# Performance work log

Hardware: AMD Instinct MI355X
Metric: run time of the kernel (lower is better)

The kernel has to match this reference:

```python
import jax, jax.numpy as jnp
import numpy as np

N_SRC0, N_DST0 = 100000, 20000   # block0: 100k src -> 20k dst
N_DST1 = 4096                    # block1: 20k src -> 4096 dst (seed nodes)


def setup_inputs() -> dict:
    key = jax.random.key(0)
    ks = jax.random.split(key, 8)
    E0, E1 = 640000, 131072
    return {
        "features": jax.random.normal(ks[0], (N_SRC0, 256), jnp.float32),
        "W1": jax.random.normal(ks[1], (256, 256), jnp.float32) * (1.0 / np.sqrt(256)),
        "b1": jnp.zeros((256,), jnp.float32),
        "W2": jax.random.normal(ks[2], (256, 128), jnp.float32) * (1.0 / np.sqrt(256)),
        "b2": jnp.zeros((128,), jnp.float32),
        "src0": jax.random.randint(ks[3], (E0,), 0, N_SRC0, jnp.int32),
        "dst0": jax.random.randint(ks[4], (E0,), 0, N_DST0, jnp.int32),
        "src1": jax.random.randint(ks[5], (E1,), 0, N_DST0, jnp.int32),
        "dst1": jax.random.randint(ks[6], (E1,), 0, N_DST1, jnp.int32),
    }


def _graph_conv(src, dst, n_dst, feat, W, b):
    # DGL GraphConv, norm='both': D_out^{-1/2} gather-sum D_in^{-1/2}, then WX+b.
    n_src = feat.shape[0]
    ones = jnp.ones(src.shape[0], feat.dtype)
    out_deg = jax.ops.segment_sum(ones, src, num_segments=n_src)
    norm_src = jnp.clip(out_deg, 1.0, None) ** -0.5          # [n_src]
    h = feat * norm_src[:, None]
    agg = jax.ops.segment_sum(h[src], dst, num_segments=n_dst)  # sparse SpMM
    in_deg = jax.ops.segment_sum(ones, dst, num_segments=n_dst)
    norm_dst = jnp.clip(in_deg, 1.0, None) ** -0.5           # [n_dst]
    return (agg * norm_dst[:, None]) @ W + b


def reference(features, W1, b1, W2, b2, src0, dst0, src1, dst1):
    x = jax.nn.relu(_graph_conv(src0, dst0, N_DST0, features, W1, b1))
    x = _graph_conv(src1, dst1, N_DST1, x, W2, b2)
    return x
```

## Files before the change

### kernel.cpp

```cpp
#include <hip/hip_runtime.h>
#include <hip/hip_bf16.h>

#define K_DIM 256
#define RSTRIDE 128
#define EPB 8192

#define G0_DB 625
#define G0_SB 256
#define G0_SW 392
#define G1_DB 128
#define G1_SB 64
#define G1_SW 313

#define NB_FIN (G0_DB + G1_DB + G0_SB + G1_SB)
#define CAST_BLKS 2048

typedef short bf16x8 __attribute__((ext_vector_type(8)));
typedef float f32x4 __attribute__((ext_vector_type(4)));

static __device__ __forceinline__ unsigned short f2bf(float x) {
    __hip_bfloat16 b = __float2bfloat16(x);
    return *reinterpret_cast<unsigned short*>(&b);
}
static __device__ __forceinline__ float bflo(unsigned int p) {
    return __uint_as_float(p << 16);
}
static __device__ __forceinline__ float bfhi(unsigned int p) {
    return __uint_as_float(p & 0xffff0000u);
}

static __device__ __forceinline__ void block_exscan(
        const int* __restrict__ hist, int* __restrict__ offs, int* __restrict__ tmp, int M) {
    const int tid = threadIdx.x;
    const int S = (M + 255) >> 8;
    const int base = tid * S;
    int sum = 0;
    for (int k = 0; k < S; ++k) {
        int idx = base + k;
        if (idx < M) sum += hist[idx];
    }
    tmp[tid] = sum;
    __syncthreads();
    for (int d = 1; d < 256; d <<= 1) {
        int v = tmp[tid];
        int u = (tid >= d) ? tmp[tid - d] : 0;
        __syncthreads();
        tmp[tid] = v + u;
        __syncthreads();
    }
    int run = (tid == 0) ? 0 : tmp[tid - 1];
    for (int k = 0; k < S; ++k) {
        int idx = base + k;
        if (idx < M) { offs[idx] = run; run += hist[idx]; }
    }
    __syncthreads();
}

struct SplitSh {
    int hist[640];
    int offs[640];
    int tmp[256];
    unsigned sorted[EPB];
};

template <int NDB, int NSB, int SW>
static __device__ __forceinline__ void split_sort(
        const int* __restrict__ src, const int* __restrict__ dst, int E, int chunk,
        int* __restrict__ cntD, int* __restrict__ offD,
        int* __restrict__ cntS, int* __restrict__ offS,
        unsigned* __restrict__ sortD, unsigned* __restrict__ sortS, SplitSh& sh) {
    const int tid = threadIdx.x;
    const int e0 = chunk * EPB;
    const int n = min(EPB, E - e0);
    for (int i = tid; i < NDB; i += 256) sh.hist[i] = 0;
    __syncthreads();
    for (int j = tid; j < n; j += 256) atomicAdd(&sh.hist[dst[e0 + j] >> 5], 1);
    __syncthreads();
    block_exscan(sh.hist, sh.offs, sh.tmp, NDB);
    for (int i = tid; i < NDB; i += 256) {
        cntD[chunk * NDB + i] = sh.hist[i];
        offD[chunk * NDB + i] = sh.offs[i];
    }
    __syncthreads();
    for (int j = tid; j < n; j += 256) {
        int d = dst[e0 + j];
        int s = src[e0 + j];
        int pos = atomicAdd(&sh.offs[d >> 5], 1);
        sh.sorted[pos] = ((unsigned)s << 5) | (unsigned)(d & 31);
    }
    __syncthreads();
    {
        unsigned* __restrict__ gout = sortD + (size_t)chunk * EPB;
        for (int j = tid; j < n; j += 256) gout[j] = sh.sorted[j];
    }
    __syncthreads();
    for (int i = tid; i < NSB; i += 256) sh.hist[i] = 0;
    __syncthreads();
    for (int j = tid; j < n; j += 256)
        atomicAdd(&sh.hist[(int)((unsigned)src[e0 + j] / SW)], 1);
    __syncthreads();
    block_exscan(sh.hist, sh.offs, sh.tmp, NSB);
    for (int i = tid; i < NSB; i += 256) {
        cntS[chunk * NSB + i] = sh.hist[i];
        offS[chunk * NSB + i] = sh.offs[i];
    }
    __syncthreads();
    for (int j = tid; j < n; j += 256) {
        unsigned s = (unsigned)src[e0 + j];
        int pos = atomicAdd(&sh.offs[s / SW], 1);
        sh.sorted[pos] = s;
    }
    __syncthreads();
    {
        unsigned* __restrict__ gout = sortS + (size_t)chunk * EPB;
        for (int j = tid; j < n; j += 256) gout[j] = sh.sorted[j];
    }
}

__global__ __launch_bounds__(256) void splitA_kernel(
        const int* __restrict__ src0, const int* __restrict__ dst0, int E0,
        const int* __restrict__ src1, const int* __restrict__ dst1, int E1,
        int* __restrict__ cntD0, int* __restrict__ offD0,
        int* __restrict__ cntS0, int* __restrict__ offS0,
        unsigned* __restrict__ sortD0, unsigned* __restrict__ sortS0,
        int* __restrict__ cntD1, int* __restrict__ offD1,
        int* __restrict__ cntS1, int* __restrict__ offS1,
        unsigned* __restrict__ sortD1, unsigned* __restrict__ sortS1,
        int nA0, int nA1,
        const float* __restrict__ W1, uint4* __restrict__ pw1,
        const float* __restrict__ W2, uint4* __restrict__ pw2) {
    __shared__ SplitSh sh;
    const int b = blockIdx.x;
    if (b < nA0) {
        split_sort<G0_DB, G0_SB, G0_SW>(src0, dst0, E0, b,
                                        cntD0, offD0, cntS0, offS0, sortD0, sortS0, sh);
    } else if (b < nA0 + nA1) {
        split_sort<G1_DB, G1_SB, G1_SW>(src1, dst1, E1, b - nA0,
                                        cntD1, offD1, cntS1, offS1, sortD1, sortS1, sh);
    } else if (b < nA0 + nA1 + 32) {
        int idx = (b - nA0 - nA1) * blockDim.x + threadIdx.x;
        int lane = idx & 63;
        int kt = (idx >> 6) & 7;
        int nt = idx >> 9;
        int n = nt * 16 + (lane & 15);
        int k = kt * 32 + (lane >> 4) * 8;
        union { unsigned short us[8]; uint4 u; } o;
#pragma unroll
        for (int j = 0; j < 8; ++j) o.us[j] = f2bf(W1[(size_t)(k + j) * 256 + n]);
        pw1[idx] = o.u;
    } else {
        int idx = (b - nA0 - nA1 - 32) * blockDim.x + threadIdx.x;
        int lane = idx & 63;
        int kt = (idx >> 6) & 7;
        int nt = idx >> 9;
        int n = nt * 16 + (lane & 15);
        int k = kt * 32 + (lane >> 4) * 8;
        union { unsigned short us[8]; uint4 u; } o;
#pragma unroll
        for (int j = 0; j < 8; ++j) o.us[j] = f2bf(W2[(size_t)(k + j) * 128 + n]);
        pw2[idx] = o.u;
    }
}

template <int NDB, int GT>
static __device__ __forceinline__ void fin_dst(
        const unsigned* __restrict__ sortD, const int* __restrict__ cntD,
        const int* __restrict__ offD, int nblk, int b,
        int* __restrict__ esrc, int* __restrict__ cnt, int* tile, int* rowc) {
    const int tid = threadIdx.x;
    if (tid < 32) rowc[tid] = 0;
    __syncthreads();
    for (int rr = tid / GT; rr < nblk; rr += 256 / GT) {
        const int c = cntD[rr * NDB + b];
        const int o = offD[rr * NDB + b];
        const unsigned* __restrict__ seg = sortD + (size_t)rr * EPB + o;
        for (int j = tid % GT; j < c; j += GT) {
            unsigned v = seg[j];
            int dloc = v & 31;
            int s = (int)(v >> 5);
            int slot = atomicAdd(&rowc[dloc], 1);
            if (slot < RSTRIDE) tile[(dloc << 7) + slot] = s;
        }
    }
    __syncthreads();
    int* __restrict__ gout = esrc + ((size_t)b << 12);
    for (int i = tid; i < 32 * RSTRIDE; i += 256) gout[i] = tile[i];
    if (tid < 32) cnt[b * 32 + tid] = rowc[tid];
}

template <int NSB, int SW, int GT>
static __device__ __forceinline__ void fin_src(
        const unsigned* __restrict__ sortS, const int* __restrict__ cntS,
        const int* __restrict__ offS, int nblk, int b, int NN,
        float* __restrict__ nv, int* hist) {
    const int tid = threadIdx.x;
    for (int i = tid; i < SW; i += 256) hist[i] = 0;
    __syncthreads();
    const int base = b * SW;
    for (int rr = tid / GT; rr < nblk; rr += 256 / GT) {
        const int c = cntS[rr * NSB + b];
        const int o = offS[rr * NSB + b];
        const unsigned* __restrict__ seg = sortS + (size_t)rr * EPB + o;
        for (int j = tid % GT; j < c; j += GT)
            atomicAdd(&hist[(int)seg[j] - base], 1);
    }
    __syncthreads();
    for (int i = tid; i < SW; i += 256) {
        int node = base + i;
        if (node < NN) nv[node] = rsqrtf((float)max(hist[i], 1));
    }
}

__global__ __launch_bounds__(256) void castfin_kernel(
        int nA0, int nA1,
        const unsigned* __restrict__ sortD0, const int* __restrict__ cntD0,
        const int* __restrict__ offD0, int* __restrict__ cnt0, int* __restrict__ esrc0,
        const unsigned* __restrict__ sortD1, const int* __restrict__ cntD1,
        const int* __restrict__ offD1, int* __restrict__ cnt1, int* __restrict__ esrc1,
        const unsigned* __restrict__ sortS0, const int* __restrict__ cntS0,
        const int* __restrict__ offS0, float* __restrict__ nv0,
        const unsigned* __restrict__ sortS1, const int* __restrict__ cntS1,
        const int* __restrict__ offS1, float* __restrict__ nv1,
        const float* __restrict__ feat, unsigned short* __restrict__ h, int numVec) {
    __shared__ union {
        struct { int tile[32 * RSTRIDE]; int rowc[32]; } d;
        int hist[G0_SW];
    } sh;
    int b = blockIdx.x;
    if (b < G0_DB) {
        fin_dst<G0_DB, 2>(sortD0, cntD0, offD0, nA0, b, esrc0, cnt0, sh.d.tile, sh.d.rowc);
    } else if (b < G0_DB + G1_DB) {
        fin_dst<G1_DB, 16>(sortD1, cntD1, offD1, nA1, b - G0_DB, esrc1, cnt1,
                           sh.d.tile, sh.d.rowc);
    } else if (b < G0_DB + G1_DB + G0_SB) {
        fin_src<G0_SB, G0_SW, 2>(sortS0, cntS0, offS0, nA0, b - G0_DB - G1_DB,
                                 100000, nv0, sh.hist);
    } else if (b < NB_FIN) {
        fin_src<G1_SB, G1_SW, 16>(sortS1, cntS1, offS1, nA1, b - G0_DB - G1_DB - G0_SB,
                                  20000, nv1, sh.hist);
    } else {
        for (int v = (b - NB_FIN) * 256 + (int)threadIdx.x; v < numVec;
             v += CAST_BLKS * 256) {
            const int idx = v * 8;
            const float4 v0 = *reinterpret_cast<const float4*>(feat + idx);
            const float4 v1 = *reinterpret_cast<const float4*>(feat + idx + 4);
            union { ushort4 u4[2]; uint4 u; } o;
            o.u4[0].x = f2bf(v0.x); o.u4[0].y = f2bf(v0.y);
            o.u4[0].z = f2bf(v0.z); o.u4[0].w = f2bf(v0.w);
            o.u4[1].x = f2bf(v1.x); o.u4[1].y = f2bf(v1.y);
            o.u4[1].z = f2bf(v1.z); o.u4[1].w = f2bf(v1.w);
            *reinterpret_cast<uint4*>(h + idx) = o.u;
        }
    }
}

template <bool NORM>
static __device__ __forceinline__ void gather2_to_lds(
        const unsigned short* __restrict__ hfeat, const int* __restrict__ esrc,
        const int* __restrict__ cnt, const float* __restrict__ nv,
        int m0, int w, int lane, unsigned short (*Alds)[264]) {
#pragma unroll
    for (int k = 0; k < 2; ++k) {
        const int rloc = w * 2 + k;
        const int row = m0 + rloc;
        const int c = cnt[row];
        const int cend = min(c, RSTRIDE);
        const int* __restrict__ ep = esrc + ((size_t)row << 7);
        float a0 = 0.f, a1 = 0.f, a2 = 0.f, a3 = 0.f;
        int i = 0;
        for (; i + 7 < cend; i += 8) {
            int s[8];
            uint2 p[8];
            float nn[8];
#pragma unroll
            for (int u = 0; u < 8; ++u) s[u] = ep[i + u];
#pragma unroll
            for (int u = 0; u < 8; ++u)
                p[u] = *reinterpret_cast<const uint2*>(hfeat + (((size_t)s[u]) << 8) + lane * 4);
#pragma unroll
            for (int u = 0; u < 8; ++u)
                nn[u] = NORM ? nv[s[u]] : 1.0f;
#pragma unroll
            for (int u = 0; u < 8; ++u) {
                if (NORM) {
                    a0 = fmaf(bflo(p[u].x), nn[u], a0); a1 = fmaf(bfhi(p[u].x), nn[u], a1);
                    a2 = fmaf(bflo(p[u].y), nn[u], a2); a3 = fmaf(bfhi(p[u].y), nn[u], a3);
                } else {
                    a0 += bflo(p[u].x); a1 += bfhi(p[u].x);
                    a2 += bflo(p[u].y); a3 += bfhi(p[u].y);
                }
            }
        }
        for (; i < cend; ++i) {
            int s0 = ep[i];
            float n0 = NORM ? nv[s0] : 1.0f;
            const uint2 p0 = *reinterpret_cast<const uint2*>(hfeat + (((size_t)s0) << 8) + lane * 4);
            if (NORM) {
                a0 = fmaf(bflo(p0.x), n0, a0); a1 = fmaf(bfhi(p0.x), n0, a1);
                a2 = fmaf(bflo(p0.y), n0, a2); a3 = fmaf(bfhi(p0.y), n0, a3);
            } else {
                a0 += bflo(p0.x); a1 += bfhi(p0.x);
                a2 += bflo(p0.y); a3 += bfhi(p0.y);
            }
        }
        float nd = rsqrtf((float)max(c, 1));
        ushort4 o;
        o.x = f2bf(a0 * nd);
        o.y = f2bf(a1 * nd);
        o.z = f2bf(a2 * nd);
        o.w = f2bf(a3 * nd);
        *reinterpret_cast<ushort4*>(&Alds[rloc][lane * 4]) = o;
    }
}

__global__ __launch_bounds__(512, 8) void fused0_kernel(
        const unsigned short* __restrict__ hfeat, const int* __restrict__ esrc,
        const int* __restrict__ cnt, const float* __restrict__ nv0,
        const uint4* __restrict__ pW, const float* __restrict__ bias,
        const float* __restrict__ nv1, unsigned short* __restrict__ out) {
    __shared__ unsigned short Alds[16][264];
    const int m0 = blockIdx.x * 16;
    const int w = threadIdx.x >> 6;
    const int lane = threadIdx.x & 63;
    gather2_to_lds<true>(hfeat, esrc, cnt, nv0, m0, w, lane, Alds);
    __syncthreads();

    bf16x8 a[8];
    const unsigned short* ap = &Alds[lane & 15][(lane >> 4) * 8];
#pragma unroll
    for (int kt = 0; kt < 8; ++kt)
        a[kt] = *reinterpret_cast<const bf16x8*>(ap + kt * 32);

    const int rbase = m0 + (lane >> 4) * 4;
    float nsv[4];
#pragma unroll
    for (int r = 0; r < 4; ++r) nsv[r] = nv1[rbase + r];

#pragma unroll
    for (int nt = 0; nt < 2; ++nt) {
        const int n0 = w * 32 + nt * 16;
        f32x4 acc = {0.f, 0.f, 0.f, 0.f};
#pragma unroll
        for (int kt = 0; kt < 8; ++kt) {
            bf16x8 b = *reinterpret_cast<const bf16x8*>(&pW[((size_t)(n0 >> 4) * 8 + kt) * 64 + lane]);
            acc = __builtin_amdgcn_mfma_f32_16x16x32_bf16(a[kt], b, acc, 0, 0, 0);
        }
        const int col = n0 + (lane & 15);
        const float bv = bias[col];
#pragma unroll
        for (int r = 0; r < 4; ++r) {
            float v = fmaxf(acc[r] + bv, 0.0f) * nsv[r];
            out[(size_t)(rbase + r) * K_DIM + col] = f2bf(v);
        }
    }
}

__global__ __launch_bounds__(512, 8) void fused1_kernel(
        const unsigned short* __restrict__ xb, const int* __restrict__ esrc,
        const int* __restrict__ cnt,
        const uint4* __restrict__ pW, const float* __restrict__ bias,
        float* __restrict__ out) {
    __shared__ unsigned short Alds[16][264];
    const int m0 = blockIdx.x * 16;
    const int w = threadIdx.x >> 6;
    const int lane = threadIdx.x & 63;
    gather2_to_lds<false>(xb, esrc, cnt, nullptr, m0, w, lane, Alds);
    __syncthreads();

    bf16x8 a[8];
    const unsigned short* ap = &Alds[lane & 15][(lane >> 4) * 8];
#pragma unroll
    for (int kt = 0; kt < 8; ++kt)
        a[kt] = *reinterpret_cast<const bf16x8*>(ap + kt * 32);

    const int rbase = m0 + (lane >> 4) * 4;
    {
        const int n0 = w * 16;
        f32x4 acc = {0.f, 0.f, 0.f, 0.f};
#pragma unroll
        for (int kt = 0; kt < 8; ++kt) {
            bf16x8 b = *reinterpret_cast<const bf16x8*>(&pW[((size_t)(n0 >> 4) * 8 + kt) * 64 + lane]);
            acc = __builtin_amdgcn_mfma_f32_16x16x32_bf16(a[kt], b, acc, 0, 0, 0);
        }
        const int col = n0 + (lane & 15);
        const float bv = bias[col];
#pragma unroll
        for (int r = 0; r < 4; ++r)
            out[(size_t)(rbase + r) * 128 + col] = acc[r] + bv;
    }
}

__global__ __launch_bounds__(256) void gatherf_kernel(
        const float* __restrict__ feat, const int* __restrict__ esrc,
        const int* __restrict__ cnt, const int* __restrict__ od,
        float* __restrict__ outbuf, int n_dst) {
    int row = blockIdx.x * (blockDim.x >> 6) + (threadIdx.x >> 6);
    int lane = threadIdx.x & 63;
    if (row >= n_dst) return;
    const int c = cnt[row];
    const int cend = min(c, RSTRIDE);
    const int* __restrict__ ep = esrc + ((size_t)row << 7);
    float4 acc = {0.f, 0.f, 0.f, 0.f};
    for (int i = 0; i < cend; ++i) {
        int s0 = ep[i];
        float n0 = rsqrtf((float)max(od[s0], 1));
        const float4 v0 = *reinterpret_cast<const float4*>(feat + (((size_t)s0) << 8) + lane * 4);
        acc.x = fmaf(v0.x, n0, acc.x); acc.y = fmaf(v0.y, n0, acc.y);
        acc.z = fmaf(v0.z, n0, acc.z); acc.w = fmaf(v0.w, n0, acc.w);
    }
    float nd = rsqrtf((float)max(c, 1));
    float4 o = {acc.x * nd, acc.y * nd, acc.z * nd, acc.w * nd};
    *reinterpret_cast<float4*>(outbuf + (((size_t)row) << 8) + lane * 4) = o;
}

__global__ void edges_kernel(const int* __restrict__ src0, const int* __restrict__ dst0,
                             int* __restrict__ od0, int* __restrict__ cnt0,
                             int* __restrict__ esrc0, int E0,
                             const int* __restrict__ src1, const int* __restrict__ dst1,
                             int* __restrict__ od1, int* __restrict__ cnt1,
                             int* __restrict__ esrc1, int E1) {
    int i = blockIdx.x * blockDim.x + threadIdx.x;
    if (i < E0) {
        int s = src0[i];
        int d = dst0[i];
        atomicAdd(&od0[s], 1);
        int slot = atomicAdd(&cnt0[d], 1);
        if (slot < RSTRIDE) esrc0[(d << 7) + slot] = s;
    } else if (i < E0 + E1) {
        int e = i - E0;
        int s = src1[e];
        int d = dst1[e];
        atomicAdd(&od1[s], 1);
        int slot = atomicAdd(&cnt1[d], 1);
        if (slot < RSTRIDE) esrc1[(d << 7) + slot] = s;
    }
}

template <int ROWS, int NCOLS, bool RELU>
__global__ __launch_bounds__(NCOLS) void gemm_kernel(
        const float* __restrict__ A, const float* __restrict__ W,
        const float* __restrict__ bias, float* __restrict__ out, int M) {
    const int row0 = blockIdx.x * ROWS;
    const int c = threadIdx.x;
    const float* __restrict__ Ablk = A + (size_t)row0 * K_DIM;
    const float* __restrict__ Wc = W + c;

    float acc[ROWS];
#pragma unroll
    for (int r = 0; r < ROWS; ++r) acc[r] = 0.0f;

    float w0 = Wc[0];
    float w1 = Wc[NCOLS];
    float w2 = Wc[2 * NCOLS];
    float w3 = Wc[3 * NCOLS];

#pragma unroll 2
    for (int k = 0; k < K_DIM - 4; k += 4) {
        const float* p = Wc + (size_t)(k + 4) * NCOLS;
        float n0 = p[0];
        float n1 = p[NCOLS];
        float n2 = p[2 * NCOLS];
        float n3 = p[3 * NCOLS];
#pragma unroll
        for (int r = 0; r < ROWS; ++r) {
            const float4 a = *reinterpret_cast<const float4*>(Ablk + r * K_DIM + k);
            acc[r] = fmaf(a.x, w0, acc[r]);
            acc[r] = fmaf(a.y, w1, acc[r]);
            acc[r] = fmaf(a.z, w2, acc[r]);
            acc[r] = fmaf(a.w, w3, acc[r]);
        }
        w0 = n0; w1 = n1; w2 = n2; w3 = n3;
    }
    {
        const int k = K_DIM - 4;
#pragma unroll
        for (int r = 0; r < ROWS; ++r) {
            const float4 a = *reinterpret_cast<const float4*>(Ablk + r * K_DIM + k);
            acc[r] = fmaf(a.x, w0, acc[r]);
            acc[r] = fmaf(a.y, w1, acc[r]);
            acc[r] = fmaf(a.z, w2, acc[r]);
            acc[r] = fmaf(a.w, w3, acc[r]);
        }
    }

    const float b = bias[c];
#pragma unroll
    for (int r = 0; r < ROWS; ++r) {
        float v = acc[r] + b;
        if (RELU) v = fmaxf(v, 0.0f);
        out[(size_t)(row0 + r) * NCOLS + c] = v;
    }
}

extern "C" void kernel_launch(void* const* d_in, const int* in_sizes, int n_in,
                              void* d_out, int out_size, void* d_ws, size_t ws_size,
                              hipStream_t stream) {
    const float* features = (const float*)d_in[0];
    const float* W1 = (const float*)d_in[1];
    const float* b1 = (const float*)d_in[2];
    const float* W2 = (const float*)d_in[3];
    const float* b2 = (const float*)d_in[4];
    const int* src0 = (const int*)d_in[5];
    const int* dst0 = (const int*)d_in[6];
    const int* src1 = (const int*)d_in[7];
    const int* dst1 = (const int*)d_in[8];
    const int E0 = in_sizes[5];
    const int E1 = in_sizes[7];
    const int NSRC0 = 100000, NDST0 = 20000, NDST1 = 4096;
    const int nA0 = (E0 + EPB - 1) / EPB;
    const int nA1 = (E1 + EPB - 1) / EPB;

    char* ws = (char*)d_ws;
    size_t off = 0;
    auto carve = [&](size_t bytes) -> void* {
        void* p = ws + off;
        off = (off + bytes + 255) & ~(size_t)255;
        return p;
    };
    int* od0  = (int*)carve((size_t)NSRC0 * 4);
    int* od1  = (int*)carve((size_t)NDST0 * 4);
    int* cnt0 = (int*)carve((size_t)NDST0 * 4);
    int* cnt1 = (int*)carve((size_t)NDST1 * 4);
    const size_t zero_span = off;
    int* esrc0p = (int*)carve((size_t)NDST0 * RSTRIDE * 4);
    int* esrc1p = (int*)carve((size_t)NDST1 * RSTRIDE * 4);
    uint4* pW1  = (uint4*)carve((size_t)8192 * 16);
    uint4* pW2  = (uint4*)carve((size_t)4096 * 16);
    int* cntD0 = (int*)carve((size_t)nA0 * G0_DB * 4);
    int* offD0 = (int*)carve((size_t)nA0 * G0_DB * 4);
    int* cntS0 = (int*)carve((size_t)nA0 * G0_SB * 4);
    int* offS0 = (int*)carve((size_t)nA0 * G0_SB * 4);
    int* cntD1 = (int*)carve((size_t)nA1 * G1_DB * 4);
    int* offD1 = (int*)carve((size_t)nA1 * G1_DB * 4);
    int* cntS1 = (int*)carve((size_t)nA1 * G1_SB * 4);
    int* offS1 = (int*)carve((size_t)nA1 * G1_SB * 4);
    unsigned* sortD0 = (unsigned*)carve((size_t)nA0 * EPB * 4);
    unsigned* sortS0 = (unsigned*)carve((size_t)nA0 * EPB * 4);
    unsigned* sortD1 = (unsigned*)carve((size_t)nA1 * EPB * 4);
    unsigned* sortS1 = (unsigned*)carve((size_t)nA1 * EPB * 4);
    unsigned short* xbufb = (unsigned short*)carve((size_t)NDST0 * K_DIM * 2);
    unsigned short* hfeat = (unsigned short*)carve((size_t)NSRC0 * K_DIM * 2);
    const size_t need_bf16 = off;
    (void)n_in; (void)out_size;

    if (ws_size >= need_bf16) {
        float* nv0 = (float*)od0;
        float* nv1 = (float*)od1;
        const int numVec = NSRC0 * K_DIM / 8;
        splitA_kernel<<<nA0 + nA1 + 48, 256, 0, stream>>>(
            src0, dst0, E0, src1, dst1, E1,
            cntD0, offD0, cntS0, offS0, sortD0, sortS0,
            cntD1, offD1, cntS1, offS1, sortD1, sortS1,
            nA0, nA1, W1, pW1, W2, pW2);
        castfin_kernel<<<NB_FIN + CAST_BLKS, 256, 0, stream>>>(
            nA0, nA1,
            sortD0, cntD0, offD0, cnt0, esrc0p,
            sortD1, cntD1, offD1, cnt1, esrc1p,
            sortS0, cntS0, offS0, nv0,
            sortS1, cntS1, offS1, nv1,
            features, hfeat, numVec);
        fused0_kernel<<<NDST0 / 16, 512, 0, stream>>>(
            hfeat, esrc0p, cnt0, nv0, pW1, b1, nv1, xbufb);
        fused1_kernel<<<NDST1 / 16, 512, 0, stream>>>(
            xbufb, esrc1p, cnt1, pW2, b2, (float*)d_out);
    } else {
        hipMemsetAsync(ws, 0, zero_span, stream);
        float* agg0 = (float*)carve((size_t)NDST0 * K_DIM * 4);
        float* xbuf = (float*)carve((size_t)NDST0 * K_DIM * 4);
        float* agg1 = (float*)carve((size_t)NDST1 * K_DIM * 4);
        edges_kernel<<<(E0 + E1 + 255) / 256, 256, 0, stream>>>(
            src0, dst0, od0, cnt0, esrc0p, E0,
            src1, dst1, od1, cnt1, esrc1p, E1);
        gatherf_kernel<<<(NDST0 + 3) / 4, 256, 0, stream>>>(features, esrc0p, cnt0, od0,
                                                            agg0, NDST0);
        gemm_kernel<16, 256, true><<<NDST0 / 16, 256, 0, stream>>>(agg0, W1, b1, xbuf, NDST0);
        gatherf_kernel<<<(NDST1 + 3) / 4, 256, 0, stream>>>(xbuf, esrc1p, cnt1, od1,
                                                            agg1, NDST1);
        gemm_kernel<4, 128, false><<<NDST1 / 4, 128, 0, stream>>>(agg1, W2, b2,
                                                                  (float*)d_out, NDST1);
    }
}
```

Measured before the change: 291.7 us.

## Use 1024-thread blocks with one wave per row; reorder cast blocks first

The fused gather+GEMM kernels now launch 1024 threads (16 waves), so each wave gathers a single destination row instead of two. In fused0 each wave also computes one 16-column MFMA tile instead of two, and in fused1 only the first 8 waves run the GEMM. The cast pass now handles 16 floats per thread and its blocks come first in the grid, ahead of the CSR finalize blocks. The goal is more memory-level parallelism in the gather and earlier scheduling of the bandwidth-heavy cast, at the cost of larger blocks, which may limit occupancy and leave half the waves idle in fused1's GEMM.

```diff
diff --git a/kernel.cpp b/kernel.cpp
--- a/kernel.cpp
+++ b/kernel.cpp
@@ -221,12 +221,34 @@
         const int* __restrict__ offS0, float* __restrict__ nv0,
         const unsigned* __restrict__ sortS1, const int* __restrict__ cntS1,
         const int* __restrict__ offS1, float* __restrict__ nv1,
-        const float* __restrict__ feat, unsigned short* __restrict__ h, int numVec) {
+        const float* __restrict__ feat, unsigned short* __restrict__ h, int numVec16) {
     __shared__ union {
         struct { int tile[32 * RSTRIDE]; int rowc[32]; } d;
         int hist[G0_SW];
     } sh;
     int b = blockIdx.x;
+    if (b < CAST_BLKS) {
+        for (int v = b * 256 + (int)threadIdx.x; v < numVec16; v += CAST_BLKS * 256) {
+            const int idx = v * 16;
+            const float4 v0 = *reinterpret_cast<const float4*>(feat + idx);
+            const float4 v1 = *reinterpret_cast<const float4*>(feat + idx + 4);
+            const float4 v2 = *reinterpret_cast<const float4*>(feat + idx + 8);
+            const float4 v3 = *reinterpret_cast<const float4*>(feat + idx + 12);
+            union { ushort4 u4[2]; uint4 u; } o01, o23;
+            o01.u4[0].x = f2bf(v0.x); o01.u4[0].y = f2bf(v0.y);
+            o01.u4[0].z = f2bf(v0.z); o01.u4[0].w = f2bf(v0.w);
+            o01.u4[1].x = f2bf(v1.x); o01.u4[1].y = f2bf(v1.y);
+            o01.u4[1].z = f2bf(v1.z); o01.u4[1].w = f2bf(v1.w);
+            o23.u4[0].x = f2bf(v2.x); o23.u4[0].y = f2bf(v2.y);
+            o23.u4[0].z = f2bf(v2.z); o23.u4[0].w = f2bf(v2.w);
+            o23.u4[1].x = f2bf(v3.x); o23.u4[1].y = f2bf(v3.y);
+            o23.u4[1].z = f2bf(v3.z); o23.u4[1].w = f2bf(v3.w);
+            *reinterpret_cast<uint4*>(h + idx) = o01.u;
+            *reinterpret_cast<uint4*>(h + idx + 8) = o23.u;
+        }
+        return;
+    }
+    b -= CAST_BLKS;
     if (b < G0_DB) {
         fin_dst<G0_DB, 2>(sortD0, cntD0, offD0, nA0, b, esrc0, cnt0, sh.d.tile, sh.d.rowc);
     } else if (b < G0_DB + G1_DB) {
@@ -235,85 +257,67 @@
     } else if (b < G0_DB + G1_DB + G0_SB) {
         fin_src<G0_SB, G0_SW, 2>(sortS0, cntS0, offS0, nA0, b - G0_DB - G1_DB,
                                  100000, nv0, sh.hist);
-    } else if (b < NB_FIN) {
+    } else {
         fin_src<G1_SB, G1_SW, 16>(sortS1, cntS1, offS1, nA1, b - G0_DB - G1_DB - G0_SB,
                                   20000, nv1, sh.hist);
-    } else {
-        for (int v = (b - NB_FIN) * 256 + (int)threadIdx.x; v < numVec;
-             v += CAST_BLKS * 256) {
-            const int idx = v * 8;
-            const float4 v0 = *reinterpret_cast<const float4*>(feat + idx);
-            const float4 v1 = *reinterpret_cast<const float4*>(feat + idx + 4);
-            union { ushort4 u4[2]; uint4 u; } o;
-            o.u4[0].x = f2bf(v0.x); o.u4[0].y = f2bf(v0.y);
-            o.u4[0].z = f2bf(v0.z); o.u4[0].w = f2bf(v0.w);
-            o.u4[1].x = f2bf(v1.x); o.u4[1].y = f2bf(v1.y);
-            o.u4[1].z = f2bf(v1.z); o.u4[1].w = f2bf(v1.w);
-            *reinterpret_cast<uint4*>(h + idx) = o.u;
-        }
     }
 }
 
 template <bool NORM>
-static __device__ __forceinline__ void gather2_to_lds(
+static __device__ __forceinline__ void gather1_to_lds(
         const unsigned short* __restrict__ hfeat, const int* __restrict__ esrc,
         const int* __restrict__ cnt, const float* __restrict__ nv,
-        int m0, int w, int lane, unsigned short (*Alds)[264]) {
-#pragma unroll
-    for (int k = 0; k < 2; ++k) {
-        const int rloc = w * 2 + k;
-        const int row = m0 + rloc;
-        const int c = cnt[row];
-        const int cend = min(c, RSTRIDE);
-        const int* __restrict__ ep = esrc + ((size_t)row << 7);
-        float a0 = 0.f, a1 = 0.f, a2 = 0.f, a3 = 0.f;
-        int i = 0;
-        for (; i + 7 < cend; i += 8) {
-            int s[8];
-            uint2 p[8];
-            float nn[8];
-#pragma unroll
-            for (int u = 0; u < 8; ++u) s[u] = ep[i + u];
-#pragma unroll
-            for (int u = 0; u < 8; ++u)
-                p[u] = *reinterpret_cast<const uint2*>(hfeat + (((size_t)s[u]) << 8) + lane * 4);
-#pragma unroll
-            for (int u = 0; u < 8; ++u)
-                nn[u] = NORM ? nv[s[u]] : 1.0f;
-#pragma unroll
-            for (int u = 0; u < 8; ++u) {
-                if (NORM) {
-                    a0 = fmaf(bflo(p[u].x), nn[u], a0); a1 = fmaf(bfhi(p[u].x), nn[u], a1);
-                    a2 = fmaf(bflo(p[u].y), nn[u], a2); a3 = fmaf(bfhi(p[u].y), nn[u], a3);
-                } else {
-                    a0 += bflo(p[u].x); a1 += bfhi(p[u].x);
-                    a2 += bflo(p[u].y); a3 += bfhi(p[u].y);
-                }
+        int row, int rloc, int lane, unsigned short (*Alds)[264]) {
+    const int c = cnt[row];
+    const int cend = min(c, RSTRIDE);
+    const int* __restrict__ ep = esrc + ((size_t)row << 7);
+    float a0 = 0.f, a1 = 0.f, a2 = 0.f, a3 = 0.f;
+    int i = 0;
+    for (; i + 7 < cend; i += 8) {
+        int s[8];
+        uint2 p[8];
+        float nn[8];
+#pragma unroll
+        for (int u = 0; u < 8; ++u) s[u] = ep[i + u];
+#pragma unroll
+        for (int u = 0; u < 8; ++u)
+            p[u] = *reinterpret_cast<const uint2*>(hfeat + (((size_t)s[u]) << 8) + lane * 4);
+#pragma unroll
+        for (int u = 0; u < 8; ++u)
+            nn[u] = NORM ? nv[s[u]] : 1.0f;
+#pragma unroll
+        for (int u = 0; u < 8; ++u) {
+            if (NORM) {
+                a0 = fmaf(bflo(p[u].x), nn[u], a0); a1 = fmaf(bfhi(p[u].x), nn[u], a1);
+                a2 = fmaf(bflo(p[u].y), nn[u], a2); a3 = fmaf(bfhi(p[u].y), nn[u], a3);
+            } else {
+                a0 += bflo(p[u].x); a1 += bfhi(p[u].x);
+                a2 += bflo(p[u].y); a3 += bfhi(p[u].y);
             }
         }
-        for (; i < cend; ++i) {
-            int s0 = ep[i];
-            float n0 = NORM ? nv[s0] : 1.0f;
-            const uint2 p0 = *reinterpret_cast<const uint2*>(hfeat + (((size_t)s0) << 8) + lane * 4);
-            if (NORM) {
-                a0 = fmaf(bflo(p0.x), n0, a0); a1 = fmaf(bfhi(p0.x), n0, a1);
-                a2 = fmaf(bflo(p0.y), n0, a2); a3 = fmaf(bfhi(p0.y), n0, a3);
-            } else {
-                a0 += bflo(p0.x); a1 += bfhi(p0.x);
-                a2 += bflo(p0.y); a3 += bfhi(p0.y);
-            }
-        }
-        float nd = rsqrtf((float)max(c, 1));
-        ushort4 o;
-        o.x = f2bf(a0 * nd);
-        o.y = f2bf(a1 * nd);
-        o.z = f2bf(a2 * nd);
-        o.w = f2bf(a3 * nd);
-        *reinterpret_cast<ushort4*>(&Alds[rloc][lane * 4]) = o;
-    }
-}
-
-__global__ __launch_bounds__(512, 8) void fused0_kernel(
+    }
+    for (; i < cend; ++i) {
+        int s0 = ep[i];
+        float n0 = NORM ? nv[s0] : 1.0f;
+        const uint2 p0 = *reinterpret_cast<const uint2*>(hfeat + (((size_t)s0) << 8) + lane * 4);
+        if (NORM) {
+            a0 = fmaf(bflo(p0.x), n0, a0); a1 = fmaf(bfhi(p0.x), n0, a1);
+            a2 = fmaf(bflo(p0.y), n0, a2); a3 = fmaf(bfhi(p0.y), n0, a3);
+        } else {
+            a0 += bflo(p0.x); a1 += bfhi(p0.x);
+            a2 += bflo(p0.y); a3 += bfhi(p0.y);
+        }
+    }
+    float nd = rsqrtf((float)max(c, 1));
+    ushort4 o;
+    o.x = f2bf(a0 * nd);
+    o.y = f2bf(a1 * nd);
+    o.z = f2bf(a2 * nd);
+    o.w = f2bf(a3 * nd);
+    *reinterpret_cast<ushort4*>(&Alds[rloc][lane * 4]) = o;
+}
+
+__global__ __launch_bounds__(1024, 4) void fused0_kernel(
         const unsigned short* __restrict__ hfeat, const int* __restrict__ esrc,
         const int* __restrict__ cnt, const float* __restrict__ nv0,
         const uint4* __restrict__ pW, const float* __restrict__ bias,
@@ -322,7 +326,7 @@
     const int m0 = blockIdx.x * 16;
     const int w = threadIdx.x >> 6;
     const int lane = threadIdx.x & 63;
-    gather2_to_lds<true>(hfeat, esrc, cnt, nv0, m0, w, lane, Alds);
+    gather1_to_lds<true>(hfeat, esrc, cnt, nv0, m0 + w, w, lane, Alds);
     __syncthreads();
 
     bf16x8 a[8];
@@ -336,26 +340,23 @@
 #pragma unroll
     for (int r = 0; r < 4; ++r) nsv[r] = nv1[rbase + r];
 
-#pragma unroll
-    for (int nt = 0; nt < 2; ++nt) {
-        const int n0 = w * 32 + nt * 16;
-        f32x4 acc = {0.f, 0.f, 0.f, 0.f};
-#pragma unroll
-        for (int kt = 0; kt < 8; ++kt) {
-            bf16x8 b = *reinterpret_cast<const bf16x8*>(&pW[((size_t)(n0 >> 4) * 8 + kt) * 64 + lane]);
-            acc = __builtin_amdgcn_mfma_f32_16x16x32_bf16(a[kt], b, acc, 0, 0, 0);
-        }
-        const int col = n0 + (lane & 15);
-        const float bv = bias[col];
-#pragma unroll
-        for (int r = 0; r < 4; ++r) {
-            float v = fmaxf(acc[r] + bv, 0.0f) * nsv[r];
-            out[(size_t)(rbase + r) * K_DIM + col] = f2bf(v);
-        }
-    }
-}
-
-__global__ __launch_bounds__(512, 8) void fused1_kernel(
+    const int n0 = w * 16;
+    f32x4 acc = {0.f, 0.f, 0.f, 0.f};
+#pragma unroll
+    for (int kt = 0; kt < 8; ++kt) {
+        bf16x8 b = *reinterpret_cast<const bf16x8*>(&pW[((size_t)(n0 >> 4) * 8 + kt) * 64 + lane]);
+        acc = __builtin_amdgcn_mfma_f32_16x16x32_bf16(a[kt], b, acc, 0, 0, 0);
+    }
+    const int col = n0 + (lane & 15);
+    const float bv = bias[col];
+#pragma unroll
+    for (int r = 0; r < 4; ++r) {
+        float v = fmaxf(acc[r] + bv, 0.0f) * nsv[r];
+        out[(size_t)(rbase + r) * K_DIM + col] = f2bf(v);
+    }
+}
+
+__global__ __launch_bounds__(1024, 4) void fused1_kernel(
         const unsigned short* __restrict__ xb, const int* __restrict__ esrc,
         const int* __restrict__ cnt,
         const uint4* __restrict__ pW, const float* __restrict__ bias,
@@ -364,17 +365,17 @@
     const int m0 = blockIdx.x * 16;
     const int w = threadIdx.x >> 6;
     const int lane = threadIdx.x & 63;
-    gather2_to_lds<false>(xb, esrc, cnt, nullptr, m0, w, lane, Alds);
-    __syncthreads();
-
-    bf16x8 a[8];
-    const unsigned short* ap = &Alds[lane & 15][(lane >> 4) * 8];
-#pragma unroll
-    for (int kt = 0; kt < 8; ++kt)
-        a[kt] = *reinterpret_cast<const bf16x8*>(ap + kt * 32);
-
-    const int rbase = m0 + (lane >> 4) * 4;
-    {
+    gather1_to_lds<false>(xb, esrc, cnt, nullptr, m0 + w, w, lane, Alds);
+    __syncthreads();
+
+    if (w < 8) {
+        bf16x8 a[8];
+        const unsigned short* ap = &Alds[lane & 15][(lane >> 4) * 8];
+#pragma unroll
+        for (int kt = 0; kt < 8; ++kt)
+            a[kt] = *reinterpret_cast<const bf16x8*>(ap + kt * 32);
+
+        const int rbase = m0 + (lane >> 4) * 4;
         const int n0 = w * 16;
         f32x4 acc = {0.f, 0.f, 0.f, 0.f};
 #pragma unroll
@@ -546,22 +547,22 @@
     if (ws_size >= need_bf16) {
         float* nv0 = (float*)od0;
         float* nv1 = (float*)od1;
-        const int numVec = NSRC0 * K_DIM / 8;
+        const int numVec16 = NSRC0 * K_DIM / 16;
         splitA_kernel<<<nA0 + nA1 + 48, 256, 0, stream>>>(
             src0, dst0, E0, src1, dst1, E1,
             cntD0, offD0, cntS0, offS0, sortD0, sortS0,
             cntD1, offD1, cntS1, offS1, sortD1, sortS1,
             nA0, nA1, W1, pW1, W2, pW2);
-        castfin_kernel<<<NB_FIN + CAST_BLKS, 256, 0, stream>>>(
+        castfin_kernel<<<CAST_BLKS + NB_FIN, 256, 0, stream>>>(
             nA0, nA1,
             sortD0, cntD0, offD0, cnt0, esrc0p,
             sortD1, cntD1, offD1, cnt1, esrc1p,
             sortS0, cntS0, offS0, nv0,
             sortS1, cntS1, offS1, nv1,
-            features, hfeat, numVec);
-        fused0_kernel<<<NDST0 / 16, 512, 0, stream>>>(
+            features, hfeat, numVec16);
+        fused0_kernel<<<NDST0 / 16, 1024, 0, stream>>>(
             hfeat, esrc0p, cnt0, nv0, pW1, b1, nv1, xbufb);
-        fused1_kernel<<<NDST1 / 16, 512, 0, stream>>>(
+        fused1_kernel<<<NDST1 / 16, 1024, 0, stream>>>(
             xbufb, esrc1p, cnt1, pW2, b2, (float*)d_out);
     } else {
         hipMemsetAsync(ws, 0, zero_span, stream);
```

Result: no change. 295.0 us (+1.1%).
